# Performance work log

Hardware: AMD Instinct MI355X
Metric: run time of the kernel (lower is better)

The kernel has to match this reference:

```python
import jax, jax.numpy as jnp
import numpy as np

N, K, DIM = 65536, 32, 64


def setup_inputs() -> dict:
    key = jax.random.key(0)
    k1, k2, k3, k4 = jax.random.split(key, 4)
    x = jax.random.normal(k1, (N, DIM), jnp.float32)
    log_pi = jax.random.normal(k2, (K, 1), jnp.float32)
    mu = jax.random.normal(k3, (K, DIM), jnp.float32)
    log_sigma_ = jax.random.normal(k4, (K, DIM, DIM), jnp.float32) / 100.0
    return {"x": x, "log_pi": log_pi, "mu": mu, "log_sigma_": log_sigma_}


def reference(x, log_pi, mu, log_sigma_):
    k, d = mu.shape
    # Faithful to torch: softmax over the size-1 last axis of (K,1) -> all ones.
    pi = jax.nn.softmax(log_pi, axis=-1)  # (K, 1)
    # scale_tril construction: strict lower triangle kept, diagonal -> exp(diag) + 1e-3
    diag = jnp.exp(jnp.diagonal(log_sigma_, axis1=-2, axis2=-1)) + 1e-3  # (K, d)
    L = jnp.tril(log_sigma_, -1) + jnp.eye(d, dtype=x.dtype) * diag[:, None, :]  # (K, d, d)
    # batched MVN log_prob via triangular solve
    diff = x[:, None, :] - mu[None, :, :]            # (N, K, d)
    b = jnp.transpose(diff, (1, 2, 0))               # (K, d, N)
    z = jax.scipy.linalg.solve_triangular(L, b, lower=True)  # (K, d, N)
    maha = jnp.sum(z * z, axis=1)                    # (K, N)
    logdet = jnp.sum(jnp.log(diag), axis=-1)         # (K,)
    logp = -0.5 * (maha + d * jnp.log(2.0 * jnp.pi)) - logdet[:, None]  # (K, N)
    p = jnp.exp(logp).T                              # (N, K)
    return jnp.log(jnp.matmul(p, pi).squeeze())      # (N,)
```

## Files before the change

kernel.cpp:

```cpp
#include <hip/hip_runtime.h>

#define KK 32
#define DD 64
#define NB 65536
#define PAD 68
#define FRAGS 6
#define SLOT (FRAGS * 64)
#define MREF 103.0f
#define L2E 1.4426950408889634f

typedef __attribute__((ext_vector_type(8))) short bf16x8;
typedef __attribute__((ext_vector_type(4))) float f32x4;

__device__ inline short f2bf(float f) {
  uint32_t u = __builtin_bit_cast(uint32_t, f);
  uint32_t r = (u + 0x7fffu + ((u >> 16) & 1u)) >> 16;
  return (short)(r & 0xffffu);
}
__device__ inline uint4 pack8(const short* v) {
  uint4 u;
  u.x = (uint32_t)(unsigned short)v[0] | ((uint32_t)(unsigned short)v[1] << 16);
  u.y = (uint32_t)(unsigned short)v[2] | ((uint32_t)(unsigned short)v[3] << 16);
  u.z = (uint32_t)(unsigned short)v[4] | ((uint32_t)(unsigned short)v[5] << 16);
  u.w = (uint32_t)(unsigned short)v[6] | ((uint32_t)(unsigned short)v[7] << 16);
  return u;
}

__device__ __forceinline__ void gl_lds16(const uint4* g, uint4* l) {
  __builtin_amdgcn_global_load_lds(
      (__attribute__((address_space(1))) void*)g,
      (__attribute__((address_space(3))) void*)l, 16, 0, 0);
}

__global__ __launch_bounds__(256) void md_prep(const float* __restrict__ ls,
                                               const float* __restrict__ mu,
                                               uint4* __restrict__ Bp,
                                               float* __restrict__ Cc,
                                               float* __restrict__ Kcl2) {
  __shared__ float Ls[DD * DD];
  __shared__ float Ys[DD * PAD];
  __shared__ float invdL[DD];
  __shared__ float muL[DD];
  const int k = blockIdx.x, t = threadIdx.x;
  const int j = t >> 2, sub = t & 3;
  const float* __restrict__ lsk = ls + (size_t)k * DD * DD;

#pragma unroll
  for (int it = 0; it < 4; ++it) {
    const int o = (it * 256 + t) * 4;
    *(float4*)&Ls[o] = *(const float4*)&lsk[o];
  }
  if (t < DD) muL[t] = mu[k * DD + t];
  __syncthreads();
  if (t < DD) invdL[t] = 1.0f / (expf(Ls[t * DD + t]) + 1e-3f);
  __syncthreads();

  const float invdj = invdL[j];
  float z[16];
#pragma unroll
  for (int mi = 0; mi < 16; ++mi) z[mi] = 0.f;
#pragma unroll
  for (int i = 0; i < DD; ++i) {
    float p = 0.f;
#pragma unroll
    for (int mi = 0; mi < 16; ++mi) {
      if (4 * mi < i) {
        const int m = 4 * mi + sub;
        p = fmaf(Ls[i * DD + m], (m < i) ? z[mi] : 0.f, p);
      }
    }
    p += __shfl_xor(p, 1, 64);
    p += __shfl_xor(p, 2, 64);
    const float zi = (i == j) ? invdj : -p * invdL[i];
    if (sub == (i & 3)) z[i >> 2] = zi;
  }
#pragma unroll
  for (int mi = 0; mi < 16; ++mi) Ys[(4 * mi + sub) * PAD + j] = z[mi];
  __syncthreads();

  {
    float p = 0.f;
#pragma unroll
    for (int mi = 0; mi < 16; ++mi) {
      const int m = 4 * mi + sub;
      p = fmaf(Ys[j * PAD + m], muL[m], p);
    }
    p += __shfl_xor(p, 1, 64);
    p += __shfl_xor(p, 2, 64);
    if (sub == 0) Cc[k * DD + j] = p;
  }

  if (t < DD) {
    float r = -logf(invdL[t]);
#pragma unroll
    for (int off = 32; off > 0; off >>= 1) r += __shfl_down(r, off, 64);
    if (t == 0)
      Kcl2[k] = (MREF - 0.5f * (64.0f * 1.83787706640934534f) - r) * L2E;
  }

  if (t < DD) {
    const int colp = t & 15, qp = t >> 4;
    uint4* slot = Bp + (size_t)k * SLOT;
#pragma unroll
    for (int s = 0; s < 2; ++s) {
#pragma unroll
      for (int ct = 0; ct < 4; ++ct) {
        if (s == 1 && ct < 2) continue;
        const int i = colp + 16 * ct;
        short hh[8];
#pragma unroll
        for (int jj = 0; jj < 8; ++jj) {
          const int m = s * 32 + qp * 8 + jj;
          const float v = Ys[i * PAD + m] - ((i == m) ? 1.0f : 0.0f);
          hh[jj] = f2bf(v);
        }
        const int fi = (s == 0) ? ct : (2 + ct);
        slot[fi * 64 + t] = pack8(hh);
      }
    }
  }
}

__global__ __launch_bounds__(256, 2) void md_main(const float* __restrict__ x,
                                                  const uint4* __restrict__ Bp,
                                                  const float* __restrict__ Cc,
                                                  const float* __restrict__ Kcl2,
                                                  float* __restrict__ out) {
  __shared__ uint4 lds4[8 * SLOT];
  __shared__ float CcL[KK * DD];
  __shared__ float sOut[2 * 128];
  const int tid = threadIdx.x, lane = tid & 63, w = tid >> 6;
  const int sg = w & 1, kg = w >> 1;
  const int sblk = blockIdx.x;
  const int base = sblk * 128 + sg * 64;
  const int k0 = kg * 16;
  const int col = lane & 15, q = lane >> 4;

  bf16x8 Xh[4][2];
#pragma unroll
  for (int Bt = 0; Bt < 4; ++Bt) {
#pragma unroll
    for (int s = 0; s < 2; ++s) {
      const float* src = x + (size_t)(base + Bt * 16 + col) * DD + s * 32 + q * 8;
      const float4 v0 = *(const float4*)src;
      const float4 v1 = *(const float4*)(src + 4);
      const float f[8] = {v0.x, v0.y, v0.z, v0.w, v1.x, v1.y, v1.z, v1.w};
      bf16x8 h;
#pragma unroll
      for (int jj = 0; jj < 8; ++jj) h[jj] = f2bf(f[jj]);
      Xh[Bt][s] = h;
    }
  }

  f32x4 xg[4][4];
#pragma unroll
  for (int ct = 0; ct < 4; ++ct)
#pragma unroll
    for (int Bt = 0; Bt < 4; ++Bt)
      xg[ct][Bt] = *(const f32x4*)&x[(size_t)(base + Bt * 16 + col) * DD +
                                     ct * 16 + q * 4];

#pragma unroll
  for (int it = 0; it < 8; ++it)
    CcL[it * 256 + tid] = Cc[it * 256 + tid];

  {
    const uint4* src = Bp + (size_t)(k0 + sg) * SLOT;
#pragma unroll
    for (int t = 0; t < 6; ++t)
      gl_lds16(src + t * 64 + lane,
               &lds4[((kg * 2 + 0) * 2 + sg) * SLOT + t * 64]);
  }
  __syncthreads();

  float run_s[4] = {0.f, 0.f, 0.f, 0.f};

#pragma unroll
  for (int kp = 0; kp < 8; ++kp) {
    const int p = kp & 1;
    if (kp < 7) {
      const uint4* src = Bp + (size_t)(k0 + 2 * (kp + 1) + sg) * SLOT;
#pragma unroll
      for (int t = 0; t < 6; ++t)
        gl_lds16(src + t * 64 + lane,
                 &lds4[((kg * 2 + (1 - p)) * 2 + sg) * SLOT + t * 64]);
    }

#pragma unroll
    for (int c = 0; c < 2; ++c) {
      const int kabs = k0 + 2 * kp + c;
      const float kc = Kcl2[kabs];
      const uint4* buf = &lds4[((kg * 2 + p) * 2 + c) * SLOT];

      f32x4 mah[4];
#pragma unroll
      for (int Bt = 0; Bt < 4; ++Bt) mah[Bt] = (f32x4){0.f, 0.f, 0.f, 0.f};

#pragma unroll
      for (int ct = 0; ct < 4; ++ct) {
        const bf16x8 A0 = *(const bf16x8*)&buf[ct * 64 + lane];
        bf16x8 A1{};
        if (ct >= 2) A1 = *(const bf16x8*)&buf[(2 + ct) * 64 + lane];
        const f32x4 cK = *(const f32x4*)&CcL[kabs * DD + ct * 16 + q * 4];
#pragma unroll
        for (int Bt = 0; Bt < 4; ++Bt) {
          f32x4 z = xg[ct][Bt];
          z = __builtin_amdgcn_mfma_f32_16x16x32_bf16(A0, Xh[Bt][0], z, 0, 0, 0);
          if (ct >= 2)
            z = __builtin_amdgcn_mfma_f32_16x16x32_bf16(A1, Xh[Bt][1], z, 0, 0, 0);
          const f32x4 d = z - cK;
          mah[Bt] += d * d;
        }
      }

#pragma unroll
      for (int Bt = 0; Bt < 4; ++Bt) {
        float s = (mah[Bt][0] + mah[Bt][1]) + (mah[Bt][2] + mah[Bt][3]);
        s += __shfl_xor(s, 16, 64);
        s += __shfl_xor(s, 32, 64);
        const float tt = fmaf(-0.5f * L2E, s, kc);
        run_s[Bt] += exp2f(tt);
      }
    }

    if (kp < 7) __syncthreads();
  }

  if (q == 0) {
#pragma unroll
    for (int Bt = 0; Bt < 4; ++Bt)
      sOut[kg * 128 + sg * 64 + Bt * 16 + col] = run_s[Bt];
  }
  __syncthreads();
  if (tid < 128) {
    const float S = sOut[tid] + sOut[128 + tid];
    out[sblk * 128 + tid] = logf(S) - MREF;
  }
}

extern "C" void kernel_launch(void* const* d_in, const int* in_sizes, int n_in,
                              void* d_out, int out_size, void* d_ws, size_t ws_size,
                              hipStream_t stream) {
  const float* x  = (const float*)d_in[0];
  const float* mu = (const float*)d_in[2];
  const float* ls = (const float*)d_in[3];
  float* out = (float*)d_out;

  char* ws = (char*)d_ws;
  uint4* Bp   = (uint4*)ws;
  float* Cc   = (float*)(ws + (size_t)KK * SLOT * 16);
  float* Kcl2 = Cc + KK * DD;

  md_prep<<<KK, 256, 0, stream>>>(ls, mu, Bp, Cc, Kcl2);
  md_main<<<NB / 128, 256, 0, stream>>>(x, Bp, Cc, Kcl2, out);
}
```

Measured before the change: 103.1 us.

## Switch main kernel from 16x16x32 to 32x32x16 bf16 MFMA tiles

Re-tiles the Mahalanobis matmul to use 32x32x16 bf16 MFMA instead of 16x16x32. The prep kernel repacks the triangular B fragments into the 32-row layout, and the main kernel reloads x operands and accumulators to match. The larger tiles cut MFMA instruction count and cross-lane shuffles (one xor instead of two) and may improve operand reuse. In exchange, 16-wide accumulators raise register pressure, and the triangular skip is now at 32-row granularity, so some zero blocks are computed.

Result: no change. 102.0 us (-1.1%).

```diff
diff --git a/kernel.cpp b/kernel.cpp
--- a/kernel.cpp
+++ b/kernel.cpp
@@ -11,6 +11,7 @@
 
 typedef __attribute__((ext_vector_type(8))) short bf16x8;
 typedef __attribute__((ext_vector_type(4))) float f32x4;
+typedef __attribute__((ext_vector_type(16))) float f32x16;
 
 __device__ inline short f2bf(float f) {
   uint32_t u = __builtin_bit_cast(uint32_t, f);
@@ -99,22 +100,22 @@
   }
 
   if (t < DD) {
-    const int colp = t & 15, qp = t >> 4;
+    const int r32 = t & 31, h = t >> 5;
     uint4* slot = Bp + (size_t)k * SLOT;
 #pragma unroll
-    for (int s = 0; s < 2; ++s) {
-#pragma unroll
-      for (int ct = 0; ct < 4; ++ct) {
-        if (s == 1 && ct < 2) continue;
-        const int i = colp + 16 * ct;
+    for (int it = 0; it < 2; ++it) {
+#pragma unroll
+      for (int kt = 0; kt < 4; ++kt) {
+        if (it == 0 && kt >= 2) continue;
+        const int i = it * 32 + r32;
         short hh[8];
 #pragma unroll
         for (int jj = 0; jj < 8; ++jj) {
-          const int m = s * 32 + qp * 8 + jj;
+          const int m = kt * 16 + h * 8 + jj;
           const float v = Ys[i * PAD + m] - ((i == m) ? 1.0f : 0.0f);
           hh[jj] = f2bf(v);
         }
-        const int fi = (s == 0) ? ct : (2 + ct);
+        const int fi = (it == 0) ? kt : (2 + kt);
         slot[fi * 64 + t] = pack8(hh);
       }
     }
@@ -134,31 +135,38 @@
   const int sblk = blockIdx.x;
   const int base = sblk * 128 + sg * 64;
   const int k0 = kg * 16;
-  const int col = lane & 15, q = lane >> 4;
-
-  bf16x8 Xh[4][2];
-#pragma unroll
-  for (int Bt = 0; Bt < 4; ++Bt) {
-#pragma unroll
-    for (int s = 0; s < 2; ++s) {
-      const float* src = x + (size_t)(base + Bt * 16 + col) * DD + s * 32 + q * 8;
+  const int c32 = lane & 31, h = lane >> 5;
+
+  bf16x8 Xb[2][4];
+#pragma unroll
+  for (int st = 0; st < 2; ++st) {
+#pragma unroll
+    for (int kt = 0; kt < 4; ++kt) {
+      const float* src = x + (size_t)(base + st * 32 + c32) * DD + kt * 16 + h * 8;
       const float4 v0 = *(const float4*)src;
       const float4 v1 = *(const float4*)(src + 4);
       const float f[8] = {v0.x, v0.y, v0.z, v0.w, v1.x, v1.y, v1.z, v1.w};
-      bf16x8 h;
-#pragma unroll
-      for (int jj = 0; jj < 8; ++jj) h[jj] = f2bf(f[jj]);
-      Xh[Bt][s] = h;
-    }
-  }
-
-  f32x4 xg[4][4];
-#pragma unroll
-  for (int ct = 0; ct < 4; ++ct)
-#pragma unroll
-    for (int Bt = 0; Bt < 4; ++Bt)
-      xg[ct][Bt] = *(const f32x4*)&x[(size_t)(base + Bt * 16 + col) * DD +
-                                     ct * 16 + q * 4];
+      bf16x8 hb;
+#pragma unroll
+      for (int jj = 0; jj < 8; ++jj) hb[jj] = f2bf(f[jj]);
+      Xb[st][kt] = hb;
+    }
+  }
+
+  f32x16 xg[2][2];
+#pragma unroll
+  for (int it = 0; it < 2; ++it)
+#pragma unroll
+    for (int st = 0; st < 2; ++st)
+#pragma unroll
+      for (int g = 0; g < 4; ++g) {
+        const f32x4 v = *(const f32x4*)&x[(size_t)(base + st * 32 + c32) * DD +
+                                          it * 32 + g * 8 + 4 * h];
+        xg[it][st][4 * g + 0] = v[0];
+        xg[it][st][4 * g + 1] = v[1];
+        xg[it][st][4 * g + 2] = v[2];
+        xg[it][st][4 * g + 3] = v[3];
+      }
 
 #pragma unroll
   for (int it = 0; it < 8; ++it)
@@ -173,7 +181,7 @@
   }
   __syncthreads();
 
-  float run_s[4] = {0.f, 0.f, 0.f, 0.f};
+  float run_s[2] = {0.f, 0.f};
 
 #pragma unroll
   for (int kp = 0; kp < 8; ++kp) {
@@ -192,44 +200,58 @@
       const float kc = Kcl2[kabs];
       const uint4* buf = &lds4[((kg * 2 + p) * 2 + c) * SLOT];
 
-      f32x4 mah[4];
-#pragma unroll
-      for (int Bt = 0; Bt < 4; ++Bt) mah[Bt] = (f32x4){0.f, 0.f, 0.f, 0.f};
-
-#pragma unroll
-      for (int ct = 0; ct < 4; ++ct) {
-        const bf16x8 A0 = *(const bf16x8*)&buf[ct * 64 + lane];
-        bf16x8 A1{};
-        if (ct >= 2) A1 = *(const bf16x8*)&buf[(2 + ct) * 64 + lane];
-        const f32x4 cK = *(const f32x4*)&CcL[kabs * DD + ct * 16 + q * 4];
-#pragma unroll
-        for (int Bt = 0; Bt < 4; ++Bt) {
-          f32x4 z = xg[ct][Bt];
-          z = __builtin_amdgcn_mfma_f32_16x16x32_bf16(A0, Xh[Bt][0], z, 0, 0, 0);
-          if (ct >= 2)
-            z = __builtin_amdgcn_mfma_f32_16x16x32_bf16(A1, Xh[Bt][1], z, 0, 0, 0);
-          const f32x4 d = z - cK;
-          mah[Bt] += d * d;
+      f32x16 cK[2];
+#pragma unroll
+      for (int it = 0; it < 2; ++it)
+#pragma unroll
+        for (int g = 0; g < 4; ++g) {
+          const f32x4 v = *(const f32x4*)&CcL[kabs * DD + it * 32 + g * 8 + 4 * h];
+          cK[it][4 * g + 0] = v[0];
+          cK[it][4 * g + 1] = v[1];
+          cK[it][4 * g + 2] = v[2];
+          cK[it][4 * g + 3] = v[3];
         }
-      }
-
-#pragma unroll
-      for (int Bt = 0; Bt < 4; ++Bt) {
-        float s = (mah[Bt][0] + mah[Bt][1]) + (mah[Bt][2] + mah[Bt][3]);
-        s += __shfl_xor(s, 16, 64);
+
+#pragma unroll
+      for (int st = 0; st < 2; ++st) {
+        f32x16 acc = (f32x16)(0.f);
+#pragma unroll
+        for (int it = 0; it < 2; ++it) {
+          f32x16 z = xg[it][st];
+          if (it == 0) {
+            const bf16x8 A0 = *(const bf16x8*)&buf[0 * 64 + lane];
+            const bf16x8 A1 = *(const bf16x8*)&buf[1 * 64 + lane];
+            z = __builtin_amdgcn_mfma_f32_32x32x16_bf16(A0, Xb[st][0], z, 0, 0, 0);
+            z = __builtin_amdgcn_mfma_f32_32x32x16_bf16(A1, Xb[st][1], z, 0, 0, 0);
+          } else {
+            const bf16x8 A0 = *(const bf16x8*)&buf[2 * 64 + lane];
+            const bf16x8 A1 = *(const bf16x8*)&buf[3 * 64 + lane];
+            const bf16x8 A2 = *(const bf16x8*)&buf[4 * 64 + lane];
+            const bf16x8 A3 = *(const bf16x8*)&buf[5 * 64 + lane];
+            z = __builtin_amdgcn_mfma_f32_32x32x16_bf16(A0, Xb[st][0], z, 0, 0, 0);
+            z = __builtin_amdgcn_mfma_f32_32x32x16_bf16(A1, Xb[st][1], z, 0, 0, 0);
+            z = __builtin_amdgcn_mfma_f32_32x32x16_bf16(A2, Xb[st][2], z, 0, 0, 0);
+            z = __builtin_amdgcn_mfma_f32_32x32x16_bf16(A3, Xb[st][3], z, 0, 0, 0);
+          }
+          const f32x16 d = z - cK[it];
+          acc += d * d;
+        }
+        float s = 0.f;
+#pragma unroll
+        for (int r = 0; r < 16; ++r) s += acc[r];
         s += __shfl_xor(s, 32, 64);
         const float tt = fmaf(-0.5f * L2E, s, kc);
-        run_s[Bt] += exp2f(tt);
+        run_s[st] += exp2f(tt);
       }
     }
 
     if (kp < 7) __syncthreads();
   }
 
-  if (q == 0) {
-#pragma unroll
-    for (int Bt = 0; Bt < 4; ++Bt)
-      sOut[kg * 128 + sg * 64 + Bt * 16 + col] = run_s[Bt];
+  if (h == 0) {
+#pragma unroll
+    for (int st = 0; st < 2; ++st)
+      sOut[kg * 128 + sg * 64 + st * 32 + c32] = run_s[st];
   }
   __syncthreads();
   if (tid < 128) {
```
